# Performance work log

Hardware: AMD Instinct MI355X
Metric: run time of the kernel (lower is better)

## Reference

```python
import jax, jax.numpy as jnp
import numpy as np
import math

DENOM = 32.0

# e3nn scalar_activation normalizes the activation to unit second moment under N(0,1).
# Compute the gelu normalization constant by Gauss-Hermite quadrature.
_zs, _ws = np.polynomial.hermite_e.hermegauss(64)
_g = 0.5 * _zs * (1.0 + np.array([math.erf(z / math.sqrt(2.0)) for z in _zs]))
C_GELU = float(1.0 / math.sqrt((_ws * _g * _g).sum() / math.sqrt(2.0 * math.pi)))


def _spherical_harmonics(r):
    # r: [E,3] unit vectors. Component-normalized real SH for l=1,2,3.
    x, y, z = r[..., 0], r[..., 1], r[..., 2]
    s3, s5, s15 = math.sqrt(3.0), math.sqrt(5.0), math.sqrt(15.0)
    s7, s105 = math.sqrt(7.0), math.sqrt(105.0)
    s35_8, s21_8 = math.sqrt(35.0 / 8.0), math.sqrt(21.0 / 8.0)
    Y1 = s3 * r                                                     # [E,3]
    Y2 = jnp.stack([s15 * x * y, s15 * y * z, 0.5 * s5 * (3 * z * z - 1),
                    s15 * x * z, 0.5 * s15 * (x * x - y * y)], -1)   # [E,5]
    Y3 = jnp.stack([s35_8 * y * (3 * x * x - y * y), s105 * x * y * z,
                    s21_8 * y * (5 * z * z - 1), 0.5 * s7 * z * (5 * z * z - 3),
                    s21_8 * x * (5 * z * z - 1), 0.5 * s105 * z * (x * x - y * y),
                    s35_8 * x * (x * x - 3 * y * y)], -1)            # [E,7]
    return [Y1, Y2, Y3]


def setup_inputs() -> dict:
    key = jax.random.key(0)
    k = jax.random.split(key, 7)
    N, E, MUL, TMUL = 32768, 1048576, 16, 32
    return {
        "x": jax.random.normal(k[0], (N, MUL), jnp.float32),
        "positions": jax.random.normal(k[1], (N, 3), jnp.float32),
        "W_pre": jax.random.normal(k[2], (4, MUL, TMUL), jnp.float32),
        "W_post": jax.random.normal(k[3], (4, TMUL, TMUL), jnp.float32),
        "W_shortcut": jax.random.normal(k[4], (MUL, TMUL), jnp.float32),
        "senders": jax.random.randint(k[5], (E,), 0, N, jnp.int32),
        "receivers": jax.random.randint(k[6], (E,), 0, N, jnp.int32),
    }


def reference(x, positions, W_pre, W_post, W_shortcut, senders, receivers):
    N, mul = x.shape
    tmul = W_pre.shape[-1]
    # --- edge update: sh of relative positions, tensor product with sender scalars ---
    rvec = positions[receivers] - positions[senders]                 # [E,3]
    n = jnp.linalg.norm(rvec, axis=-1, keepdims=True)
    rhat = rvec / jnp.where(n == 0, 1.0, n)
    Ys = _spherical_harmonics(rhat)
    s = x[senders]                                                   # [E,mul] (0e)
    # --- aggregate edge features at receivers (segment sum) ---
    agg = [jax.ops.segment_sum(s, receivers, num_segments=N)]        # 0e block
    for Y in Ys:
        e = (s[:, :, None] * Y[:, None, :]).reshape(s.shape[0], -1)  # 0e x l -> l
        agg.append(jax.ops.segment_sum(e, receivers, num_segments=N).reshape(N, mul, Y.shape[-1]))
    # --- node update: linear_pre -> scalar act -> linear_post, plus shortcut ---
    inv_in = 1.0 / math.sqrt(mul)
    inv_mid = 1.0 / math.sqrt(tmul)
    out = []
    for l in range(4):
        a = agg[l] / DENOM
        if l == 0:
            p = (a @ W_pre[0]) * inv_in
            p = C_GELU * jax.nn.gelu(p, approximate=False)           # act on 0e scalars only
            q = (p @ W_post[0]) * inv_mid
            q = q + (x @ W_shortcut) * inv_in                        # shortcut: only 0e path exists
            out.append(q)
        else:
            p = jnp.einsum('nui,uv->nvi', a, W_pre[l]) * inv_in
            q = jnp.einsum('nvi,vw->nwi', p, W_post[l]) * inv_mid
            out.append(q.reshape(N, -1))
    return jnp.concatenate(out, axis=-1)                              # [N, tmul*16]
```

## Files before the change

### kernel.cpp

```cpp
#include <hip/hip_runtime.h>
#include <math.h>

#define NN 32768
#define EN 1048576
#define NBIN 256
#define BINCAP 8192
#define TILE 4096

#define C_GELU_F 1.5335262f

__global__ __launch_bounds__(512) void bin_k(const int* __restrict__ snd,
                                             const int* __restrict__ rcv,
                                             const float* __restrict__ pos,
                                             float4* __restrict__ posw,
                                             int* __restrict__ bin_cur,
                                             unsigned* __restrict__ binbuf) {
    __shared__ unsigned cnt[NBIN];
    __shared__ unsigned excl[NBIN];
    __shared__ unsigned cur2[NBIN];
    __shared__ unsigned gbase[NBIN];
    __shared__ unsigned stage[TILE];
    int t = threadIdx.x;
    int tile = blockIdx.x * TILE;
    if (t < NBIN) { cnt[t] = 0; cur2[t] = 0; }
    if (t < 128) {
        int n = (blockIdx.x << 7) + t;
        posw[n] = make_float4(pos[3*n], pos[3*n+1], pos[3*n+2], 0.f);
    }
    __syncthreads();

    unsigned w[TILE / 512];
#pragma unroll
    for (int i = 0; i < TILE / 512; ++i) {
        int e = tile + i * 512 + t;
        unsigned r = (unsigned)rcv[e], s = (unsigned)snd[e];
        w[i] = (r << 15) | s;
        atomicAdd(&cnt[w[i] >> 22], 1u);
    }
    __syncthreads();

    unsigned my = (t < NBIN) ? cnt[t] : 0u;
    if (t < NBIN) excl[t] = my;
    __syncthreads();
    for (int d = 1; d < NBIN; d <<= 1) {
        unsigned v = (t < NBIN && t >= d) ? excl[t - d] : 0u;
        __syncthreads();
        if (t < NBIN) excl[t] += v;
        __syncthreads();
    }
    if (t < NBIN) {
        unsigned myexcl = excl[t] - my;
        gbase[t] = atomicAdd((unsigned*)&bin_cur[t], my);
        excl[t] = myexcl;
    }
    __syncthreads();

#pragma unroll
    for (int i = 0; i < TILE / 512; ++i) {
        unsigned b = w[i] >> 22;
        unsigned p = excl[b] + atomicAdd(&cur2[b], 1u);
        stage[p] = w[i];
    }
    __syncthreads();

    for (int p = t; p < TILE; p += 512) {
        unsigned ww = stage[p];
        unsigned b = ww >> 22;
        unsigned idx = gbase[b] + ((unsigned)p - excl[b]);
        if (idx < BINCAP) binbuf[b * BINCAP + idx] = ww;
    }
}

__global__ __launch_bounds__(1024) void csr_k(const int* __restrict__ bin_cur,
                                              const unsigned* __restrict__ binbuf,
                                              int* __restrict__ row_ptr,
                                              int* __restrict__ edge_csr) {
    __shared__ unsigned sc[NBIN];
    __shared__ unsigned cnt[128];
    __shared__ unsigned excl[128];
    __shared__ unsigned cur2[128];
    int b = blockIdx.x;
    int t = threadIdx.x;

    if (t < NBIN) sc[t] = (unsigned)bin_cur[t];
    __syncthreads();
    for (int d = 1; d < NBIN; d <<= 1) {
        unsigned v = (t < NBIN && t >= d) ? sc[t - d] : 0u;
        __syncthreads();
        if (t < NBIN) sc[t] += v;
        __syncthreads();
    }
    int Mraw = bin_cur[b];
    int base = (int)(sc[b] - (unsigned)Mraw);
    int M = Mraw > BINCAP ? BINCAP : Mraw;
    if (t < 128) { cnt[t] = 0; cur2[t] = 0; }
    __syncthreads();

    const unsigned* bb = binbuf + b * BINCAP;
    for (int i = t; i < M; i += 1024)
        atomicAdd(&cnt[(bb[i] >> 15) & 127], 1u);
    __syncthreads();

    if (t < 128) excl[t] = cnt[t];
    __syncthreads();
    for (int d = 1; d < 128; d <<= 1) {
        unsigned v = (t >= d && t < 128) ? excl[t - d] : 0u;
        __syncthreads();
        if (t < 128) excl[t] += v;
        __syncthreads();
    }
    if (t < 128) {
        unsigned e = excl[t] - cnt[t];
        excl[t] = e;
        row_ptr[(b << 7) + t] = base + (int)e;
        if (b == NBIN - 1 && t == 127) row_ptr[NN] = base + (int)(e + cnt[127]);
    }
    __syncthreads();

    for (int i = t; i < M; i += 1024) {
        unsigned ww = bb[i];
        unsigned r7 = (ww >> 15) & 127;
        unsigned dst = excl[r7] + atomicAdd(&cur2[r7], 1u);
        edge_csr[base + dst] = (int)(ww & 0x7FFF);
    }
}

#define GROUPS 32
#define BLK 512
#define YST 20
#define GST (16*YST + 8)

__global__ __launch_bounds__(512, 4) void fused_k(const float* __restrict__ x,
                                                  const float4* __restrict__ posw,
                                                  const int* __restrict__ row_ptr,
                                                  const int* __restrict__ edge_csr,
                                                  const float* __restrict__ Wpre,
                                                  const float* __restrict__ Wpost,
                                                  const float* __restrict__ Wsc,
                                                  float* __restrict__ out) {
    __shared__ float sPre[4*516];
    __shared__ float sPost[4*1028];
    __shared__ float sSc[512];
    __shared__ float sY[GROUPS * GST];

    int t = threadIdx.x;
    for (int idx = t; idx < 2048; idx += BLK)
        sPre[(idx >> 9)*516 + (idx & 511)] = Wpre[idx];
    for (int idx = t; idx < 4096; idx += BLK)
        sPost[(idx >> 10)*1028 + (idx & 1023)] = Wpost[idx];
    sSc[t] = Wsc[t];
    __syncthreads();

    int g = t >> 4;
    int j = t & 15;
    int n = blockIdx.x * GROUPS + g;
    int beg = row_ptr[n], end = row_ptr[n + 1];
    int cnt = end - beg;
    float4 rp = posw[n];
    float* yg = sY + g * GST;

    const float s3   = 1.7320508075688772f;
    const float s5   = 2.2360679774997896f;
    const float s15  = 3.8729833462074170f;
    const float s7   = 2.6457513110645907f;
    const float s105 = 10.246950765959598f;
    const float s35_8 = 2.0916500663351889f;
    const float s21_8 = 1.6201851746019651f;

    float acc[16];
#pragma unroll
    for (int u = 0; u < 16; ++u) acc[u] = 0.f;

    int nch = (cnt + 15) >> 4;
    if (nch > 0) {
        int ki0 = (j < cnt) ? j : cnt - 1;
        int sE = edge_csr[beg + ki0];
        float4 sp = posw[sE];

        for (int c = 0; c < nch; ++c) {
            int kn = ((c + 1) << 4) + j;
            int kiN = (kn < cnt) ? kn : cnt - 1;
            int sEn = edge_csr[beg + kiN];

            float vx = rp.x - sp.x, vy = rp.y - sp.y, vz = rp.z - sp.z;
            float n2 = vx*vx + vy*vy + vz*vz;
            float inv;
            if (n2 > 0.f) {
                inv = rsqrtf(n2);
                inv = inv * (1.5f - 0.5f * n2 * inv * inv);
            } else inv = 0.f;
            float X = vx*inv, Y = vy*inv, Z = vz*inv;
            float XX = X*X, YY = Y*Y, ZZ = Z*Z;
            float m = (((c << 4) + j) < cnt) ? 1.f : 0.f;

            float* yr = yg + j * YST;
            ((float4*)yr)[0] = make_float4(m, m*(s3*X), m*(s3*Y), m*(s3*Z));
            ((float4*)yr)[1] = make_float4(m*(s15*X*Y), m*(s15*Y*Z),
                                           m*(0.5f*s5*(3.f*ZZ - 1.f)), m*(s15*X*Z));
            ((float4*)yr)[2] = make_float4(m*(0.5f*s15*(XX - YY)),
                                           m*(s35_8*Y*(3.f*XX - YY)),
                                           m*(s105*X*Y*Z),
                                           m*(s21_8*Y*(5.f*ZZ - 1.f)));
            ((float4*)yr)[3] = make_float4(m*(0.5f*s7*Z*(5.f*ZZ - 3.f)),
                                           m*(s21_8*X*(5.f*ZZ - 1.f)),
                                           m*(0.5f*s105*Z*(XX - YY)),
                                           m*(s35_8*X*(XX - 3.f*YY)));

            int se[16];
#pragma unroll
            for (int e = 0; e < 16; ++e)
                se[e] = __shfl(sE, (t & 48) + e, 64);
            float yt[16];
#pragma unroll
            for (int e = 0; e < 16; ++e)
                yt[e] = yg[e * YST + j];

            float4 spn = posw[sEn];

#pragma unroll
            for (int e = 0; e < 16; ++e) {
                float y = yt[e];
                const float4* xp = (const float4*)(x + (se[e] << 4));
                float4 a0 = xp[0], a1 = xp[1], a2 = xp[2], a3 = xp[3];
                acc[0]  += a0.x * y;  acc[1]  += a0.y * y;
                acc[2]  += a0.z * y;  acc[3]  += a0.w * y;
                acc[4]  += a1.x * y;  acc[5]  += a1.y * y;
                acc[6]  += a1.z * y;  acc[7]  += a1.w * y;
                acc[8]  += a2.x * y;  acc[9]  += a2.y * y;
                acc[10] += a2.z * y;  acc[11] += a2.w * y;
                acc[12] += a3.x * y;  acc[13] += a3.y * y;
                acc[14] += a3.z * y;  acc[15] += a3.w * y;
            }

            sE = sEn; sp = spn;
        }
    }

    int l, i, offl, deg;
    if (j == 0)      { l = 0; i = 0;     offl = 0;   deg = 1; }
    else if (j < 4)  { l = 1; i = j - 1; offl = 32;  deg = 3; }
    else if (j < 9)  { l = 2; i = j - 4; offl = 128; deg = 5; }
    else             { l = 3; i = j - 9; offl = 288; deg = 7; }

    const float c1 = 0.0078125f;
    const float c2 = 0.17677669529663687f;

    float p[32];
#pragma unroll
    for (int v = 0; v < 32; ++v) p[v] = 0.f;
    const float* wp = sPre + l * 516;
#pragma unroll
    for (int uu = 0; uu < 16; ++uu) {
        float a = acc[uu];
        const float4* w4 = (const float4*)(wp + (uu << 5));
#pragma unroll
        for (int vq = 0; vq < 8; ++vq) {
            float4 w = w4[vq];
            p[4*vq+0] += a * w.x;
            p[4*vq+1] += a * w.y;
            p[4*vq+2] += a * w.z;
            p[4*vq+3] += a * w.w;
        }
    }
#pragma unroll
    for (int v = 0; v < 32; ++v) p[v] *= c1;

    if (j == 0) {
#pragma unroll
        for (int v = 0; v < 32; ++v) {
            float pv = p[v];
            p[v] = C_GELU_F * 0.5f * pv * (1.f + erff(pv * 0.7071067811865476f));
        }
    }

    float q[32];
#pragma unroll
    for (int w = 0; w < 32; ++w) q[w] = 0.f;
    const float* wq = sPost + l * 1028;
#pragma unroll
    for (int v = 0; v < 32; ++v) {
        float pv = p[v];
        const float4* w4 = (const float4*)(wq + (v << 5));
#pragma unroll
        for (int wd = 0; wd < 8; ++wd) {
            float4 w = w4[wd];
            q[4*wd+0] += pv * w.x;
            q[4*wd+1] += pv * w.y;
            q[4*wd+2] += pv * w.z;
            q[4*wd+3] += pv * w.w;
        }
    }
#pragma unroll
    for (int w = 0; w < 32; ++w) q[w] *= c2;

    if (j == 0) {
        const float* xp = x + (n << 4);
#pragma unroll
        for (int uu = 0; uu < 16; ++uu) {
            float xv = 0.25f * xp[uu];
            const float4* w4 = (const float4*)(sSc + (uu << 5));
#pragma unroll
            for (int wd = 0; wd < 8; ++wd) {
                float4 w = w4[wd];
                q[4*wd+0] += xv * w.x;
                q[4*wd+1] += xv * w.y;
                q[4*wd+2] += xv * w.z;
                q[4*wd+3] += xv * w.w;
            }
        }
    }

    float* op = out + (n << 9) + offl + i;
#pragma unroll
    for (int w = 0; w < 32; ++w) op[w * deg] = q[w];
}

extern "C" void kernel_launch(void* const* d_in, const int* in_sizes, int n_in,
                              void* d_out, int out_size, void* d_ws, size_t ws_size,
                              hipStream_t stream) {
    const float* x     = (const float*)d_in[0];
    const float* pos   = (const float*)d_in[1];
    const float* Wpre  = (const float*)d_in[2];
    const float* Wpost = (const float*)d_in[3];
    const float* Wsc   = (const float*)d_in[4];
    const int*   snd   = (const int*)d_in[5];
    const int*   rcv   = (const int*)d_in[6];
    float* out = (float*)d_out;

    char* ws = (char*)d_ws;
    int*      bin_cur   = (int*)(ws);
    int*      row_ptr   = (int*)(ws + 2048);
    float4*   posw      = (float4*)(ws + 0x30000);
    int*      edge_csr  = (int*)(ws + 0xB0000);
    unsigned* binbuf    = (unsigned*)(ws + 0x500000);

    hipMemsetAsync(bin_cur, 0, NBIN * sizeof(int), stream);
    bin_k<<<EN / TILE, 512, 0, stream>>>(snd, rcv, pos, posw, bin_cur, binbuf);
    csr_k<<<NBIN, 1024, 0, stream>>>(bin_cur, binbuf, row_ptr, edge_csr);
    fused_k<<<NN / GROUPS, BLK, 0, stream>>>(x, posw, row_ptr, edge_csr,
                                             Wpre, Wpost, Wsc, out);
}
```

Baseline: 186.1 us.

## Replace binned CSR build with atomic histogram/scatter and shrink fused blocks

Replaces the two-pass bin-then-sort CSR construction with a global atomic histogram, a wave-level scan assigning per-node offsets, and an atomic scatter that leaves edges unordered within each node. The fused kernel moves to 256-thread blocks with a higher occupancy hint, drops the shared-memory copies of the weight matrices in favour of direct global or cached loads, and spreads the GELU of the scalar path across all lanes through shared memory. The aim is fewer sync-heavy preprocessing passes, less shared memory per block, and less divergence in the GELU step. The costs are heavy global atomic contention in the histogram and scatter, edge order that changes from run to run and so can change the floating-point summation order, and weight reads that now come from global memory instead of LDS.

```diff
diff --git a/kernel.cpp b/kernel.cpp
--- a/kernel.cpp
+++ b/kernel.cpp
@@ -3,159 +3,86 @@
 
 #define NN 32768
 #define EN 1048576
-#define NBIN 256
-#define BINCAP 8192
-#define TILE 4096
 
 #define C_GELU_F 1.5335262f
 
-__global__ __launch_bounds__(512) void bin_k(const int* __restrict__ snd,
-                                             const int* __restrict__ rcv,
-                                             const float* __restrict__ pos,
-                                             float4* __restrict__ posw,
-                                             int* __restrict__ bin_cur,
-                                             unsigned* __restrict__ binbuf) {
-    __shared__ unsigned cnt[NBIN];
-    __shared__ unsigned excl[NBIN];
-    __shared__ unsigned cur2[NBIN];
-    __shared__ unsigned gbase[NBIN];
-    __shared__ unsigned stage[TILE];
-    int t = threadIdx.x;
-    int tile = blockIdx.x * TILE;
-    if (t < NBIN) { cnt[t] = 0; cur2[t] = 0; }
-    if (t < 128) {
-        int n = (blockIdx.x << 7) + t;
-        posw[n] = make_float4(pos[3*n], pos[3*n+1], pos[3*n+2], 0.f);
-    }
-    __syncthreads();
-
-    unsigned w[TILE / 512];
-#pragma unroll
-    for (int i = 0; i < TILE / 512; ++i) {
-        int e = tile + i * 512 + t;
-        unsigned r = (unsigned)rcv[e], s = (unsigned)snd[e];
-        w[i] = (r << 15) | s;
-        atomicAdd(&cnt[w[i] >> 22], 1u);
-    }
-    __syncthreads();
-
-    unsigned my = (t < NBIN) ? cnt[t] : 0u;
-    if (t < NBIN) excl[t] = my;
-    __syncthreads();
-    for (int d = 1; d < NBIN; d <<= 1) {
-        unsigned v = (t < NBIN && t >= d) ? excl[t - d] : 0u;
-        __syncthreads();
-        if (t < NBIN) excl[t] += v;
-        __syncthreads();
-    }
-    if (t < NBIN) {
-        unsigned myexcl = excl[t] - my;
-        gbase[t] = atomicAdd((unsigned*)&bin_cur[t], my);
-        excl[t] = myexcl;
-    }
-    __syncthreads();
-
-#pragma unroll
-    for (int i = 0; i < TILE / 512; ++i) {
-        unsigned b = w[i] >> 22;
-        unsigned p = excl[b] + atomicAdd(&cur2[b], 1u);
-        stage[p] = w[i];
-    }
-    __syncthreads();
-
-    for (int p = t; p < TILE; p += 512) {
-        unsigned ww = stage[p];
-        unsigned b = ww >> 22;
-        unsigned idx = gbase[b] + ((unsigned)p - excl[b]);
-        if (idx < BINCAP) binbuf[b * BINCAP + idx] = ww;
-    }
-}
-
-__global__ __launch_bounds__(1024) void csr_k(const int* __restrict__ bin_cur,
-                                              const unsigned* __restrict__ binbuf,
-                                              int* __restrict__ row_ptr,
-                                              int* __restrict__ edge_csr) {
-    __shared__ unsigned sc[NBIN];
-    __shared__ unsigned cnt[128];
-    __shared__ unsigned excl[128];
-    __shared__ unsigned cur2[128];
-    int b = blockIdx.x;
-    int t = threadIdx.x;
-
-    if (t < NBIN) sc[t] = (unsigned)bin_cur[t];
-    __syncthreads();
-    for (int d = 1; d < NBIN; d <<= 1) {
-        unsigned v = (t < NBIN && t >= d) ? sc[t - d] : 0u;
-        __syncthreads();
-        if (t < NBIN) sc[t] += v;
-        __syncthreads();
-    }
-    int Mraw = bin_cur[b];
-    int base = (int)(sc[b] - (unsigned)Mraw);
-    int M = Mraw > BINCAP ? BINCAP : Mraw;
-    if (t < 128) { cnt[t] = 0; cur2[t] = 0; }
-    __syncthreads();
-
-    const unsigned* bb = binbuf + b * BINCAP;
-    for (int i = t; i < M; i += 1024)
-        atomicAdd(&cnt[(bb[i] >> 15) & 127], 1u);
-    __syncthreads();
-
-    if (t < 128) excl[t] = cnt[t];
-    __syncthreads();
-    for (int d = 1; d < 128; d <<= 1) {
-        unsigned v = (t >= d && t < 128) ? excl[t - d] : 0u;
-        __syncthreads();
-        if (t < 128) excl[t] += v;
-        __syncthreads();
-    }
-    if (t < 128) {
-        unsigned e = excl[t] - cnt[t];
-        excl[t] = e;
-        row_ptr[(b << 7) + t] = base + (int)e;
-        if (b == NBIN - 1 && t == 127) row_ptr[NN] = base + (int)(e + cnt[127]);
-    }
-    __syncthreads();
-
-    for (int i = t; i < M; i += 1024) {
-        unsigned ww = bb[i];
-        unsigned r7 = (ww >> 15) & 127;
-        unsigned dst = excl[r7] + atomicAdd(&cur2[r7], 1u);
-        edge_csr[base + dst] = (int)(ww & 0x7FFF);
-    }
-}
-
-#define GROUPS 32
-#define BLK 512
+__global__ __launch_bounds__(256) void hist_k(const int* __restrict__ rcv,
+                                              const float* __restrict__ pos,
+                                              float4* __restrict__ posw,
+                                              int* __restrict__ cnt) {
+    int tid = blockIdx.x * 256 + threadIdx.x;
+    if (tid < NN)
+        posw[tid] = make_float4(pos[3*tid], pos[3*tid+1], pos[3*tid+2], 0.f);
+    for (int e = tid; e < EN; e += 256 * 256)
+        atomicAdd(&cnt[rcv[e]], 1);
+}
+
+__global__ __launch_bounds__(512) void assign_k(const int* __restrict__ cnt,
+                                                unsigned* __restrict__ cursor,
+                                                int* __restrict__ beg) {
+    int t = blockIdx.x * 512 + threadIdx.x;
+    int wid = t >> 6;
+    int lane = t & 63;
+    int rbase = wid << 9;
+    unsigned c[8]; unsigned sum = 0;
+#pragma unroll
+    for (int k = 0; k < 8; ++k) {
+        c[k] = (unsigned)cnt[rbase + (k << 6) + lane];
+        sum += c[k];
+    }
+    unsigned s = sum;
+#pragma unroll
+    for (int d = 1; d < 64; d <<= 1) {
+        unsigned v = __shfl_up(s, d, 64);
+        if (lane >= d) s += v;
+    }
+    unsigned tot = __shfl(s, 63, 64);
+    unsigned base0 = 0;
+    if (lane == 63) base0 = atomicAdd(cursor, tot);
+    base0 = __shfl(base0, 63, 64);
+    unsigned my = base0 + (s - sum);
+#pragma unroll
+    for (int k = 0; k < 8; ++k) {
+        beg[rbase + (k << 6) + lane] = (int)my;
+        my += c[k];
+    }
+}
+
+__global__ __launch_bounds__(256) void scatter_k(const int* __restrict__ snd,
+                                                 const int* __restrict__ rcv,
+                                                 const int* __restrict__ beg,
+                                                 int* __restrict__ cur,
+                                                 int* __restrict__ edge_csr) {
+    int tid = blockIdx.x * 256 + threadIdx.x;
+    for (int e = tid; e < EN; e += 256 * 256) {
+        int r = rcv[e];
+        int o = atomicAdd(&cur[r], 1);
+        edge_csr[beg[r] + o] = snd[e];
+    }
+}
+
+#define GROUPS 16
+#define BLK 256
 #define YST 20
 #define GST (16*YST + 8)
 
-__global__ __launch_bounds__(512, 4) void fused_k(const float* __restrict__ x,
+__global__ __launch_bounds__(256, 6) void fused_k(const float* __restrict__ x,
                                                   const float4* __restrict__ posw,
-                                                  const int* __restrict__ row_ptr,
+                                                  const int* __restrict__ begA,
+                                                  const int* __restrict__ cntA,
                                                   const int* __restrict__ edge_csr,
                                                   const float* __restrict__ Wpre,
                                                   const float* __restrict__ Wpost,
                                                   const float* __restrict__ Wsc,
                                                   float* __restrict__ out) {
-    __shared__ float sPre[4*516];
-    __shared__ float sPost[4*1028];
-    __shared__ float sSc[512];
     __shared__ float sY[GROUPS * GST];
 
     int t = threadIdx.x;
-    for (int idx = t; idx < 2048; idx += BLK)
-        sPre[(idx >> 9)*516 + (idx & 511)] = Wpre[idx];
-    for (int idx = t; idx < 4096; idx += BLK)
-        sPost[(idx >> 10)*1028 + (idx & 1023)] = Wpost[idx];
-    sSc[t] = Wsc[t];
-    __syncthreads();
-
     int g = t >> 4;
     int j = t & 15;
     int n = blockIdx.x * GROUPS + g;
-    int beg = row_ptr[n], end = row_ptr[n + 1];
-    int cnt = end - beg;
+    int beg = begA[n];
+    int cnt = cntA[n];
     float4 rp = posw[n];
     float* yg = sY + g * GST;
 
@@ -248,7 +175,7 @@
     float p[32];
 #pragma unroll
     for (int v = 0; v < 32; ++v) p[v] = 0.f;
-    const float* wp = sPre + l * 516;
+    const float* wp = Wpre + (l << 9);
 #pragma unroll
     for (int uu = 0; uu < 16; ++uu) {
         float a = acc[uu];
@@ -265,18 +192,39 @@
 #pragma unroll
     for (int v = 0; v < 32; ++v) p[v] *= c1;
 
-    if (j == 0) {
-#pragma unroll
-        for (int v = 0; v < 32; ++v) {
-            float pv = p[v];
-            p[v] = C_GELU_F * 0.5f * pv * (1.f + erff(pv * 0.7071067811865476f));
+    {
+        int lane = t & 63;
+        int gw4 = (t >> 6) << 2;
+        if (j == 0) {
+            float* pg = sY + g * GST;
+#pragma unroll
+            for (int k8 = 0; k8 < 8; ++k8)
+                ((float4*)pg)[k8] = make_float4(p[4*k8], p[4*k8+1],
+                                                p[4*k8+2], p[4*k8+3]);
+        }
+#pragma unroll
+        for (int pass = 0; pass < 2; ++pass) {
+            int idx = (pass << 6) + lane;
+            float* ad = sY + (gw4 + (idx >> 5)) * GST + (idx & 31);
+            float tv = *ad;
+            tv = C_GELU_F * 0.5f * tv * (1.f + erff(tv * 0.7071067811865476f));
+            *ad = tv;
+        }
+        if (j == 0) {
+            float* pg = sY + g * GST;
+#pragma unroll
+            for (int k8 = 0; k8 < 8; ++k8) {
+                float4 gg = ((const float4*)pg)[k8];
+                p[4*k8]   = gg.x; p[4*k8+1] = gg.y;
+                p[4*k8+2] = gg.z; p[4*k8+3] = gg.w;
+            }
         }
     }
 
     float q[32];
 #pragma unroll
     for (int w = 0; w < 32; ++w) q[w] = 0.f;
-    const float* wq = sPost + l * 1028;
+    const float* wq = Wpost + (l << 10);
 #pragma unroll
     for (int v = 0; v < 32; ++v) {
         float pv = p[v];
@@ -298,7 +246,7 @@
 #pragma unroll
         for (int uu = 0; uu < 16; ++uu) {
             float xv = 0.25f * xp[uu];
-            const float4* w4 = (const float4*)(sSc + (uu << 5));
+            const float4* w4 = (const float4*)(Wsc + (uu << 5));
 #pragma unroll
             for (int wd = 0; wd < 8; ++wd) {
                 float4 w = w4[wd];
@@ -328,15 +276,17 @@
     float* out = (float*)d_out;
 
     char* ws = (char*)d_ws;
-    int*      bin_cur   = (int*)(ws);
-    int*      row_ptr   = (int*)(ws + 2048);
-    float4*   posw      = (float4*)(ws + 0x30000);
-    int*      edge_csr  = (int*)(ws + 0xB0000);
-    unsigned* binbuf    = (unsigned*)(ws + 0x500000);
-
-    hipMemsetAsync(bin_cur, 0, NBIN * sizeof(int), stream);
-    bin_k<<<EN / TILE, 512, 0, stream>>>(snd, rcv, pos, posw, bin_cur, binbuf);
-    csr_k<<<NBIN, 1024, 0, stream>>>(bin_cur, binbuf, row_ptr, edge_csr);
-    fused_k<<<NN / GROUPS, BLK, 0, stream>>>(x, posw, row_ptr, edge_csr,
+    int*      cnt      = (int*)(ws);
+    int*      cur      = (int*)(ws + 0x20000);
+    unsigned* cursor   = (unsigned*)(ws + 0x40000);
+    int*      beg      = (int*)(ws + 0x50000);
+    float4*   posw     = (float4*)(ws + 0x80000);
+    int*      edge_csr = (int*)(ws + 0x100000);
+
+    hipMemsetAsync(ws, 0, 0x40010, stream);
+    hist_k<<<256, 256, 0, stream>>>(rcv, pos, posw, cnt);
+    assign_k<<<8, 512, 0, stream>>>(cnt, cursor, beg);
+    scatter_k<<<256, 256, 0, stream>>>(snd, rcv, beg, cur, edge_csr);
+    fused_k<<<NN / GROUPS, BLK, 0, stream>>>(x, posw, beg, cnt, edge_csr,
                                              Wpre, Wpost, Wsc, out);
 }
```

Result: slower. 411.7 us (+121.2%).
